# Optimization experiments

Measured on AMD Instinct MI355X. Metric: run time of the kernel, lower is better.

## Reference

```python
import jax, jax.numpy as jnp
import numpy as np

N_NODES = 4096
N_EDGES = 8192
N_GRAPHS = 256
D_NODE = 64
D_EDGE = 32
H = 256


def setup_inputs() -> dict:
    key = jax.random.key(0)
    ks = jax.random.split(key, 16)
    s = lambda d: 1.0 / np.sqrt(d)
    inp = {
        "x": jax.random.normal(ks[0], (N_NODES, D_NODE), dtype=jnp.float32),
        "edge_index": jax.random.randint(ks[1], (2, N_EDGES), 0, N_NODES),
        "edge_attr": jax.random.normal(ks[2], (N_EDGES, D_EDGE), dtype=jnp.float32),
        "batch": jnp.sort(jax.random.randint(ks[3], (N_NODES,), 0, N_GRAPHS)),
        # conv1: edge MLP 32 -> 64*256, root weight 64->256, bias 256
        "nn1_w": jax.random.normal(ks[4], (D_EDGE, D_NODE * H), dtype=jnp.float32) * s(D_EDGE),
        "nn1_b": jnp.zeros((D_NODE * H,), dtype=jnp.float32),
        "root1_w": jax.random.normal(ks[5], (D_NODE, H), dtype=jnp.float32) * s(D_NODE),
        "bias1": jnp.zeros((H,), dtype=jnp.float32),
        # conv2: edge MLP 32 -> 256*256, root weight 256->256, bias 256
        "nn2_w": jax.random.normal(ks[6], (D_EDGE, H * H), dtype=jnp.float32) * s(D_EDGE),
        "nn2_b": jnp.zeros((H * H,), dtype=jnp.float32),
        "root2_w": jax.random.normal(ks[7], (H, H), dtype=jnp.float32) * s(H),
        "bias2": jnp.zeros((H,), dtype=jnp.float32),
        # readout MLP: 256 -> 128 -> 1
        "lin1_w": jax.random.normal(ks[8], (H, H // 2), dtype=jnp.float32) * s(H),
        "lin1_b": jnp.zeros((H // 2,), dtype=jnp.float32),
        "lin2_w": jax.random.normal(ks[9], (H // 2, 1), dtype=jnp.float32) * s(H // 2),
        "lin2_b": jnp.zeros((1,), dtype=jnp.float32),
    }
    return inp


def nnconv(x, src, dst, edge_attr, nn_w, nn_b, root_w, bias, out_c):
    # PyG NNConv (aggr='add'): per-edge weight matrix from edge MLP,
    # message = x[src] @ W_e, scatter-add at dst, plus root transform + bias.
    e = edge_attr.shape[0]
    in_c = x.shape[1]
    w_e = (edge_attr @ nn_w + nn_b).reshape(e, in_c, out_c)  # [E, in, out]
    msg = jnp.einsum('ei,eio->eo', x[src], w_e)              # [E, out]
    agg = jax.ops.segment_sum(msg, dst, num_segments=x.shape[0])
    return agg + x @ root_w + bias


def reference(x, edge_index, edge_attr, batch,
              nn1_w, nn1_b, root1_w, bias1,
              nn2_w, nn2_b, root2_w, bias2,
              lin1_w, lin1_b, lin2_w, lin2_b):
    src, dst = edge_index[0], edge_index[1]
    h = nnconv(x, src, dst, edge_attr, nn1_w, nn1_b, root1_w, bias1, H)
    h = jax.nn.relu(h)
    h = nnconv(h, src, dst, edge_attr, nn2_w, nn2_b, root2_w, bias2, H)
    # global mean pool over graphs
    sums = jax.ops.segment_sum(h, batch, num_segments=N_GRAPHS)
    cnts = jax.ops.segment_sum(jnp.ones((h.shape[0],), h.dtype), batch, num_segments=N_GRAPHS)
    pooled = sums / jnp.maximum(cnts, 1.0)[:, None]
    # dropout is identity in eval mode
    z = jax.nn.relu(pooled @ lin1_w + lin1_b)
    return jax.nn.sigmoid(z @ lin2_w + lin2_b)  # [N_GRAPHS, 1]
```

## Files before the change

### kernel.cpp

```cpp
#include <hip/hip_runtime.h>
#include <math.h>

#define N_NODES 4096
#define N_EDGES 8192
#define N_GRAPHS 256
#define D_NODE 64
#define D_EDGE 32
#define HH 256

#define K1 2176
#define K2 8704
#define NC1 34
#define NC2 136
#define NSL1 8
#define NSL3 32
#define CHUNK 128

typedef _Float16 half8v __attribute__((ext_vector_type(8)));
typedef _Float16 half4v __attribute__((ext_vector_type(4)));
typedef float floatx4 __attribute__((ext_vector_type(4)));

static const size_t OFF_S    = 0;
static const size_t OFF_BT1  = 17825792;
static const size_t OFF_BT2  = 18104320;
static const size_t OFF_CP   = 19218432;
static const size_t OFF_H    = 25509888;
static const size_t OFF_INT  = 26034176;

__device__ void csr_body(const int* __restrict__ dst,
                         int* __restrict__ starts,
                         int* __restrict__ elist) {
    __shared__ int cnt[4096];
    __shared__ int ps[256];
    int t = threadIdx.x;
#pragma unroll
    for (int i = 0; i < 16; ++i) cnt[t * 16 + i] = 0;
    __syncthreads();
#pragma unroll
    for (int i = 0; i < 32; ++i) atomicAdd(&cnt[dst[i * 256 + t]], 1);
    __syncthreads();
    int v[16]; int s = 0;
#pragma unroll
    for (int i = 0; i < 16; ++i) { v[i] = cnt[t * 16 + i]; s += v[i]; }
    ps[t] = s;
    __syncthreads();
    for (int off = 1; off < 256; off <<= 1) {
        int tv = (t >= off) ? ps[t - off] : 0;
        __syncthreads();
        ps[t] += tv;
        __syncthreads();
    }
    int excl = ps[t] - s;
#pragma unroll
    for (int i = 0; i < 16; ++i) {
        starts[t * 16 + i] = excl;
        cnt[t * 16 + i] = excl;
        excl += v[i];
    }
    if (t == 255) starts[4096] = excl;
    __syncthreads();
#pragma unroll
    for (int i = 0; i < 32; ++i) {
        int e = i * 256 + t;
        int d = dst[e];
        int p = atomicAdd(&cnt[d], 1);
        elist[p] = e;
    }
}

__device__ void packT_body(const float* __restrict__ w,
                           const float* __restrict__ b,
                           const float* __restrict__ rw,
                           _Float16* __restrict__ BT,
                           int kk0, int o0, int K,
                           int wlim, int blim, int wshift, int wmask, int wrow) {
    __shared__ float T[64][65];
    int t = threadIdx.x;
    int ol = t & 63, kb = t >> 6;
#pragma unroll
    for (int p = 0; p < 16; ++p) {
        int kl = p * 4 + kb;
        int kk = kk0 + kl, o = o0 + ol;
        float v;
        if (kk < wlim)      v = w[(kk >> wshift) * wrow + (kk & wmask) * 256 + o];
        else if (kk < blim) v = b[(kk - wlim) * 256 + o];
        else                v = rw[(kk - blim) * 256 + o];
        T[kl][ol] = v;
    }
    __syncthreads();
    int kl2 = t & 63, ob = t >> 6;
#pragma unroll
    for (int p = 0; p < 16; ++p) {
        int ol2 = p * 4 + ob;
        BT[(size_t)(o0 + ol2) * K + kk0 + kl2] = (_Float16)T[kl2][ol2];
    }
}

__global__ __launch_bounds__(256) void prep_k(const int* __restrict__ dst,
                                              int* __restrict__ starts,
                                              int* __restrict__ elist,
                                              const float* __restrict__ w1,
                                              const float* __restrict__ b1,
                                              const float* __restrict__ r1,
                                              const float* __restrict__ w2,
                                              const float* __restrict__ b2,
                                              const float* __restrict__ r2,
                                              _Float16* __restrict__ BT1,
                                              _Float16* __restrict__ BT2) {
    int bx = blockIdx.x, by = blockIdx.y;
    if (bx == 0) {
        if (by == 0) csr_body(dst, starts, elist);
        return;
    }
    int pbx = bx - 1, o0 = by * 64;
    if (pbx < NC1)
        packT_body(w1, b1, r1, BT1, pbx * 64, o0, K1, 2048, 2112, 6, 63, 16384);
    else
        packT_body(w2, b2, r2, BT2, (pbx - NC1) * 64, o0, K2, 8192, 8448, 8, 255, 65536);
}

__global__ __launch_bounds__(64) void s1_k(const float* __restrict__ x,
                                           const float* __restrict__ ea,
                                           const int* __restrict__ src,
                                           const int* __restrict__ starts,
                                           const int* __restrict__ elist,
                                           _Float16* __restrict__ S) {
    int n = blockIdx.x, t = threadIdx.x;
    int cg = t & 7, kg = t >> 3;
    int i0 = cg * 8;
    float acc[5][8] = {};
    int e0 = starts[n], e1 = starts[n + 1];
    for (int ie = e0; ie < e1; ++ie) {
        int e = elist[ie];
        int sn = src[e];
        float4 f0 = *(const float4*)&x[sn * 64 + i0];
        float4 f1 = *(const float4*)&x[sn * 64 + i0 + 4];
        float xv[8] = {f0.x, f0.y, f0.z, f0.w, f1.x, f1.y, f1.z, f1.w};
#pragma unroll
        for (int j = 0; j < 4; ++j) {
            float va = ea[e * 32 + kg + 8 * j];
#pragma unroll
            for (int c = 0; c < 8; ++c) acc[j][c] += va * xv[c];
        }
        if (kg == 0) {
#pragma unroll
            for (int c = 0; c < 8; ++c) acc[4][c] += xv[c];
        }
    }
    _Float16* row = S + (size_t)n * K1;
#pragma unroll
    for (int j = 0; j < 4; ++j) {
        int k = kg + 8 * j;
        half8v o;
#pragma unroll
        for (int c = 0; c < 8; ++c) o[c] = (_Float16)acc[j][c];
        *(half8v*)&row[k * 64 + i0] = o;
    }
    if (kg == 0) {
        half8v o;
#pragma unroll
        for (int c = 0; c < 8; ++c) o[c] = (_Float16)acc[4][c];
        *(half8v*)&row[32 * 64 + i0] = o;
    }
    if (kg == 1) {
        float4 f0 = *(const float4*)&x[n * 64 + i0];
        float4 f1 = *(const float4*)&x[n * 64 + i0 + 4];
        half8v o;
        o[0] = (_Float16)f0.x; o[1] = (_Float16)f0.y; o[2] = (_Float16)f0.z; o[3] = (_Float16)f0.w;
        o[4] = (_Float16)f1.x; o[5] = (_Float16)f1.y; o[6] = (_Float16)f1.z; o[7] = (_Float16)f1.w;
        *(half8v*)&row[2112 + i0] = o;
    }
}

__device__ __forceinline__ void async_copy16(const void* g, void* l) {
    __builtin_amdgcn_global_load_lds(
        (__attribute__((address_space(1))) unsigned int*)(g),
        (__attribute__((address_space(3))) unsigned int*)(l), 16, 0, 0);
}

__global__ __launch_bounds__(256, 3) void gemm_f16(const _Float16* __restrict__ A,
                                                   const _Float16* __restrict__ BT,
                                                   _Float16* __restrict__ Cpart,
                                                   int K, int NC, int Z) {
    __shared__ _Float16 lds[17408];
    _Float16* As = lds;
    _Float16* Bs = lds + 128 * 64;
    int tid = threadIdx.x;
    int w = tid >> 6, l = tid & 63;
    int mt = blockIdx.y, nt = blockIdx.x, z = blockIdx.z;
    int c0 = z * NC / Z, c1 = (z + 1) * NC / Z;
    int k0 = c0 * 64;
    int wm = w & 1, wn = w >> 1;

    int lr = l >> 3, lc = l & 7;
    int gc = lc ^ lr;
    const _Float16* gA0 = A  + (size_t)(mt * 128 + w * 32 + lr) * K + k0 + gc * 8;
    const _Float16* gB0 = BT + (size_t)(nt * 128 + w * 32 + lr) * K + k0 + gc * 8;

    int lm = l & 15, q4 = l >> 4;
    int sw = lm & 7;

    floatx4 acc[4][4] = {};

    for (int s = c0; s < c1; ++s) {
#pragma unroll
        for (int q = 0; q < 4; ++q) {
            async_copy16(gA0 + (size_t)q * 8 * K, As + (w * 32 + q * 8) * 64);
            async_copy16(gB0 + (size_t)q * 8 * K, Bs + (w * 32 + q * 8) * 64);
        }
        gA0 += 64; gB0 += 64;
        __syncthreads();
#pragma unroll
        for (int kw = 0; kw < 2; ++kw) {
            int ck = ((kw * 4 + q4) ^ sw) * 8;
            half8v af[4], bf[4];
#pragma unroll
            for (int i = 0; i < 4; ++i)
                af[i] = *(const half8v*)&As[(wm * 64 + i * 16 + lm) * 64 + ck];
#pragma unroll
            for (int j = 0; j < 4; ++j)
                bf[j] = *(const half8v*)&Bs[(wn * 64 + j * 16 + lm) * 64 + ck];
#pragma unroll
            for (int i = 0; i < 4; ++i)
#pragma unroll
                for (int j = 0; j < 4; ++j)
                    acc[i][j] = __builtin_amdgcn_mfma_f32_16x16x32_f16(af[i], bf[j], acc[i][j], 0, 0, 0);
        }
        __syncthreads();
    }

    _Float16* ep = lds + w * 4352;
#pragma unroll
    for (int i = 0; i < 4; ++i)
#pragma unroll
        for (int j = 0; j < 4; ++j)
#pragma unroll
            for (int r = 0; r < 4; ++r)
                ep[(i * 16 + q4 * 4 + r) * 68 + j * 16 + lm] = (_Float16)acc[i][j][r];
    __syncthreads();
    _Float16* Cp = Cpart + (size_t)z * (N_NODES * HH);
    int row8 = l >> 3, colg = (l & 7) * 8;
    int gm0 = mt * 128 + wm * 64, gn0 = nt * 128 + wn * 64;
#pragma unroll
    for (int i8 = 0; i8 < 8; ++i8) {
        int rr = i8 * 8 + row8;
        half4v lo = *(const half4v*)&ep[rr * 68 + colg];
        half4v hi = *(const half4v*)&ep[rr * 68 + colg + 4];
        half8v v;
        v[0] = lo[0]; v[1] = lo[1]; v[2] = lo[2]; v[3] = lo[3];
        v[4] = hi[0]; v[5] = hi[1]; v[6] = hi[2]; v[7] = hi[3];
        *(half8v*)&Cp[(size_t)(gm0 + rr) * HH + gn0 + colg] = v;
    }
}

__global__ __launch_bounds__(256) void hep_k(const _Float16* __restrict__ Cp,
                                             const float* __restrict__ bias,
                                             _Float16* __restrict__ h) {
    int idx = (blockIdx.x * 256 + threadIdx.x) * 8;
    float a[8] = {};
#pragma unroll
    for (int zz = 0; zz < NSL1; ++zz) {
        half8v v = *(const half8v*)(Cp + (size_t)zz * (N_NODES * HH) + idx);
#pragma unroll
        for (int j = 0; j < 8; ++j) a[j] += (float)v[j];
    }
    int col = idx & 255;
    half8v o;
#pragma unroll
    for (int j = 0; j < 8; ++j) o[j] = (_Float16)fmaxf(a[j] + bias[col + j], 0.f);
    *(half8v*)(h + idx) = o;
}

__global__ __launch_bounds__(256) void sg_k(const _Float16* __restrict__ h,
                                            const float* __restrict__ ea,
                                            const int* __restrict__ src,
                                            const int* __restrict__ starts,
                                            const int* __restrict__ elist,
                                            const int* __restrict__ batch,
                                            _Float16* __restrict__ SG) {
    int g = blockIdx.x, kg = blockIdx.y, t = threadIdx.x;
    __shared__ int bnds[2];
    __shared__ int sl[CHUNK];
    __shared__ int el[CHUNK];
    if (t < 2) {
        int target = g + t;
        int lo = 0, hi = N_NODES;
        while (lo < hi) { int mid = (lo + hi) >> 1; if (batch[mid] < target) lo = mid + 1; else hi = mid; }
        bnds[t] = lo;
    }
    __syncthreads();
    int nlo = bnds[0], nhi = bnds[1];
    int e0 = starts[nlo], e1 = starts[nhi];
    _Float16* row = SG + (size_t)g * K2;

    if (kg < 8) {
        float acc[4] = {};
        for (int base = e0; base < e1; base += CHUNK) {
            int ne = min(CHUNK, e1 - base);
            if (t < ne) { int e = elist[base + t]; el[t] = e; sl[t] = src[e]; }
            __syncthreads();
            int ie = 0;
            for (; ie + 8 <= ne; ie += 8) {
                float hv[8]; float4 ev[8];
#pragma unroll
                for (int u = 0; u < 8; ++u) hv[u] = (float)h[(size_t)sl[ie + u] * 256 + t];
#pragma unroll
                for (int u = 0; u < 8; ++u) ev[u] = *(const float4*)&ea[(size_t)el[ie + u] * 32 + kg * 4];
#pragma unroll
                for (int u = 0; u < 8; ++u) {
                    acc[0] += ev[u].x * hv[u]; acc[1] += ev[u].y * hv[u];
                    acc[2] += ev[u].z * hv[u]; acc[3] += ev[u].w * hv[u];
                }
            }
            for (; ie < ne; ++ie) {
                float hv = (float)h[(size_t)sl[ie] * 256 + t];
                float4 ev = *(const float4*)&ea[(size_t)el[ie] * 32 + kg * 4];
                acc[0] += ev.x * hv; acc[1] += ev.y * hv;
                acc[2] += ev.z * hv; acc[3] += ev.w * hv;
            }
            __syncthreads();
        }
#pragma unroll
        for (int j = 0; j < 4; ++j)
            row[(kg * 4 + j) * 256 + t] = (_Float16)acc[j];
    } else {
        float a32 = 0.f;
        for (int base = e0; base < e1; base += CHUNK) {
            int ne = min(CHUNK, e1 - base);
            if (t < ne) sl[t] = src[elist[base + t]];
            __syncthreads();
            int ie = 0;
            for (; ie + 8 <= ne; ie += 8) {
                float hv[8];
#pragma unroll
                for (int u = 0; u < 8; ++u) hv[u] = (float)h[(size_t)sl[ie + u] * 256 + t];
#pragma unroll
                for (int u = 0; u < 8; ++u) a32 += hv[u];
            }
            for (; ie < ne; ++ie)
                a32 += (float)h[(size_t)sl[ie] * 256 + t];
            __syncthreads();
        }
        float aug = 0.f;
        int n = nlo;
        for (; n + 4 <= nhi; n += 4) {
            float hv[4];
#pragma unroll
            for (int u = 0; u < 4; ++u) hv[u] = (float)h[(size_t)(n + u) * 256 + t];
#pragma unroll
            for (int u = 0; u < 4; ++u) aug += hv[u];
        }
        for (; n < nhi; ++n) aug += (float)h[(size_t)n * 256 + t];
        row[32 * 256 + t] = (_Float16)a32;
        row[8448 + t] = (_Float16)aug;
    }
}

__global__ __launch_bounds__(256, 3) void gemm_sg(const _Float16* __restrict__ A,
                                                  const _Float16* __restrict__ BT,
                                                  float* __restrict__ Cp,
                                                  int K, int NC, int Z) {
    __shared__ _Float16 lds[16384];
    _Float16* As = lds;
    _Float16* Bs = lds + 128 * 64;
    int tid = threadIdx.x;
    int w = tid >> 6, l = tid & 63;
    int mt = blockIdx.y, nt = blockIdx.x, z = blockIdx.z;
    int c0 = z * NC / Z, c1 = (z + 1) * NC / Z;
    int k0 = c0 * 64;
    int wm = w & 1, wn = w >> 1;

    int lr = l >> 3, lc = l & 7;
    int gc = lc ^ lr;
    const _Float16* gA0 = A  + (size_t)(mt * 128 + w * 32 + lr) * K + k0 + gc * 8;
    const _Float16* gB0 = BT + (size_t)(nt * 128 + w * 32 + lr) * K + k0 + gc * 8;

    int lm = l & 15, q4 = l >> 4;
    int sw = lm & 7;

    floatx4 acc[4][4] = {};

    for (int s = c0; s < c1; ++s) {
#pragma unroll
        for (int q = 0; q < 4; ++q) {
            async_copy16(gA0 + (size_t)q * 8 * K, As + (w * 32 + q * 8) * 64);
            async_copy16(gB0 + (size_t)q * 8 * K, Bs + (w * 32 + q * 8) * 64);
        }
        gA0 += 64; gB0 += 64;
        __syncthreads();
#pragma unroll
        for (int kw = 0; kw < 2; ++kw) {
            int ck = ((kw * 4 + q4) ^ sw) * 8;
            half8v af[4], bf[4];
#pragma unroll
            for (int i = 0; i < 4; ++i)
                af[i] = *(const half8v*)&As[(wm * 64 + i * 16 + lm) * 64 + ck];
#pragma unroll
            for (int j = 0; j < 4; ++j)
                bf[j] = *(const half8v*)&Bs[(wn * 64 + j * 16 + lm) * 64 + ck];
#pragma unroll
            for (int i = 0; i < 4; ++i)
#pragma unroll
                for (int j = 0; j < 4; ++j)
                    acc[i][j] = __builtin_amdgcn_mfma_f32_16x16x32_f16(af[i], bf[j], acc[i][j], 0, 0, 0);
        }
        __syncthreads();
    }

    float* C = Cp + (size_t)z * (N_GRAPHS * HH);
    int gm0 = mt * 128 + wm * 64, gn0 = nt * 128 + wn * 64;
#pragma unroll
    for (int i = 0; i < 4; ++i)
#pragma unroll
        for (int j = 0; j < 4; ++j)
#pragma unroll
            for (int r = 0; r < 4; ++r)
                C[(size_t)(gm0 + i * 16 + q4 * 4 + r) * HH + gn0 + j * 16 + lm] = acc[i][j][r];
}

__global__ __launch_bounds__(256) void readout_k(const float* __restrict__ CpS,
                                                 const int* __restrict__ batch,
                                                 const float* __restrict__ bias2,
                                                 const float* __restrict__ l1w,
                                                 const float* __restrict__ l1b,
                                                 const float* __restrict__ l2w,
                                                 const float* __restrict__ l2b,
                                                 float* __restrict__ out) {
    int g = blockIdx.x, t = threadIdx.x;
    __shared__ int bnds[2];
    __shared__ float sp[256];
    __shared__ float sz[128];
    if (t < 2) {
        int target = g + t;
        int lo = 0, hi = N_NODES;
        while (lo < hi) { int mid = (lo + hi) >> 1; if (batch[mid] < target) lo = mid + 1; else hi = mid; }
        bnds[t] = lo;
    }
    __syncthreads();
    int lo = bnds[0], hi = bnds[1];
    float s = 0.f;
#pragma unroll
    for (int zz = 0; zz < NSL3; ++zz)
        s += CpS[(size_t)zz * (N_GRAPHS * HH) + g * 256 + t];
    sp[t] = (hi > lo) ? (s / (float)(hi - lo) + bias2[t]) : 0.f;
    __syncthreads();
    if (t < 128) {
        float a = l1b[t];
#pragma unroll 8
        for (int i = 0; i < 256; ++i) a += sp[i] * l1w[i * 128 + t];
        sz[t] = fmaxf(a, 0.f) * l2w[t];
    }
    __syncthreads();
    for (int ss = 64; ss > 0; ss >>= 1) {
        if (t < ss) sz[t] += sz[t + ss];
        __syncthreads();
    }
    if (t == 0) {
        float zz = sz[0] + l2b[0];
        out[g] = 1.0f / (1.0f + expf(-zz));
    }
}

extern "C" void kernel_launch(void* const* d_in, const int* in_sizes, int n_in,
                              void* d_out, int out_size, void* d_ws, size_t ws_size,
                              hipStream_t stream) {
    const float* x       = (const float*)d_in[0];
    const int*   ei      = (const int*)d_in[1];
    const float* ea      = (const float*)d_in[2];
    const int*   batch   = (const int*)d_in[3];
    const float* nn1_w   = (const float*)d_in[4];
    const float* nn1_b   = (const float*)d_in[5];
    const float* root1_w = (const float*)d_in[6];
    const float* bias1   = (const float*)d_in[7];
    const float* nn2_w   = (const float*)d_in[8];
    const float* nn2_b   = (const float*)d_in[9];
    const float* root2_w = (const float*)d_in[10];
    const float* bias2   = (const float*)d_in[11];
    const float* lin1_w  = (const float*)d_in[12];
    const float* lin1_b  = (const float*)d_in[13];
    const float* lin2_w  = (const float*)d_in[14];
    const float* lin2_b  = (const float*)d_in[15];
    float* out = (float*)d_out;
    float* ws  = (float*)d_ws;

    _Float16* S   = (_Float16*)(ws + OFF_S);
    _Float16* BT1 = (_Float16*)(ws + OFF_BT1);
    _Float16* BT2 = (_Float16*)(ws + OFF_BT2);
    _Float16* Cp  = (_Float16*)(ws + OFF_CP);
    float*    CpS = ws + OFF_CP;
    _Float16* h   = (_Float16*)(ws + OFF_H);
    int* ip     = (int*)(ws + OFF_INT);
    int* starts = ip;
    int* elist  = ip + 4100;

    const int* srcv = ei;
    const int* dstv = ei + N_EDGES;

    prep_k<<<dim3(1 + NC1 + NC2, 4), 256, 0, stream>>>(
        dstv, starts, elist, nn1_w, nn1_b, root1_w, nn2_w, nn2_b, root2_w, BT1, BT2);

    s1_k<<<4096, 64, 0, stream>>>(x, ea, srcv, starts, elist, S);

    gemm_f16<<<dim3(2, 32, NSL1), 256, 0, stream>>>(S, BT1, Cp, K1, NC1, NSL1);

    hep_k<<<512, 256, 0, stream>>>(Cp, bias1, h);

    sg_k<<<dim3(N_GRAPHS, 9), 256, 0, stream>>>(h, ea, srcv, starts, elist, batch, S);

    gemm_sg<<<dim3(2, 2, NSL3), 256, 0, stream>>>(S, BT2, CpS, K2, NC2, NSL3);

    readout_k<<<N_GRAPHS, 256, 0, stream>>>(CpS, batch, bias2,
                                            lin1_w, lin1_b, lin2_w, lin2_b, out);
}
```

Measured before the change: 173.6 us.

## Precompute graph bounds, atomically pool gemm_sg output, restructure sg_k and s1_k blocks

Graph start offsets are now computed once in the prep kernel instead of by binary search in sg_k and readout_k. gemm_sg accumulates its split-K partials directly into a pool buffer with atomicAdd, with the buffer zeroed in hep_k, so the 32-slice partial buffer and its reduction in readout_k go away. sg_k now runs 2 k-slices instead of 9. Each block stages edge attributes in shared memory with a smaller chunk and accumulates 16 columns per thread. s1_k packs four nodes per 256-thread block. The trade-offs are float atomic contention and nondeterministic summation order, plus fewer blocks and higher register pressure in sg_k.

```diff
diff --git a/kernel.cpp b/kernel.cpp
--- a/kernel.cpp
+++ b/kernel.cpp
@@ -14,7 +14,7 @@
 #define NC2 136
 #define NSL1 8
 #define NSL3 32
-#define CHUNK 128
+#define CHUNK 64
 
 typedef _Float16 half8v __attribute__((ext_vector_type(8)));
 typedef _Float16 half4v __attribute__((ext_vector_type(4)));
@@ -26,6 +26,7 @@
 static const size_t OFF_CP   = 19218432;
 static const size_t OFF_H    = 25509888;
 static const size_t OFF_INT  = 26034176;
+static const size_t OFF_POOL = 26050560;
 
 __device__ void csr_body(const int* __restrict__ dst,
                          int* __restrict__ starts,
@@ -66,6 +67,14 @@
         int p = atomicAdd(&cnt[d], 1);
         elist[p] = e;
     }
+}
+
+__device__ void gstarts_body(const int* __restrict__ batch, int* __restrict__ gstarts) {
+    int t = threadIdx.x;
+    int lo = 0, hi = N_NODES;
+    while (lo < hi) { int mid = (lo + hi) >> 1; if (batch[mid] < t) lo = mid + 1; else hi = mid; }
+    gstarts[t] = lo;
+    if (t == 0) gstarts[N_GRAPHS] = N_NODES;
 }
 
 __device__ void packT_body(const float* __restrict__ w,
@@ -97,8 +106,10 @@
 }
 
 __global__ __launch_bounds__(256) void prep_k(const int* __restrict__ dst,
+                                              const int* __restrict__ batch,
                                               int* __restrict__ starts,
                                               int* __restrict__ elist,
+                                              int* __restrict__ gstarts,
                                               const float* __restrict__ w1,
                                               const float* __restrict__ b1,
                                               const float* __restrict__ r1,
@@ -110,6 +121,7 @@
     int bx = blockIdx.x, by = blockIdx.y;
     if (bx == 0) {
         if (by == 0) csr_body(dst, starts, elist);
+        else if (by == 1) gstarts_body(batch, gstarts);
         return;
     }
     int pbx = bx - 1, o0 = by * 64;
@@ -119,14 +131,16 @@
         packT_body(w2, b2, r2, BT2, (pbx - NC1) * 64, o0, K2, 8192, 8448, 8, 255, 65536);
 }
 
-__global__ __launch_bounds__(64) void s1_k(const float* __restrict__ x,
-                                           const float* __restrict__ ea,
-                                           const int* __restrict__ src,
-                                           const int* __restrict__ starts,
-                                           const int* __restrict__ elist,
-                                           _Float16* __restrict__ S) {
-    int n = blockIdx.x, t = threadIdx.x;
-    int cg = t & 7, kg = t >> 3;
+__global__ __launch_bounds__(256) void s1_k(const float* __restrict__ x,
+                                            const float* __restrict__ ea,
+                                            const int* __restrict__ src,
+                                            const int* __restrict__ starts,
+                                            const int* __restrict__ elist,
+                                            _Float16* __restrict__ S) {
+    int t = threadIdx.x;
+    int n = blockIdx.x * 4 + (t >> 6);
+    int tl = t & 63;
+    int cg = tl & 7, kg = tl >> 3;
     int i0 = cg * 8;
     float acc[5][8] = {};
     int e0 = starts[n], e1 = starts[n + 1];
@@ -255,7 +269,9 @@
 
 __global__ __launch_bounds__(256) void hep_k(const _Float16* __restrict__ Cp,
                                              const float* __restrict__ bias,
-                                             _Float16* __restrict__ h) {
+                                             _Float16* __restrict__ h,
+                                             float* __restrict__ pool) {
+    if (blockIdx.x < 256) pool[blockIdx.x * 256 + threadIdx.x] = 0.f;
     int idx = (blockIdx.x * 256 + threadIdx.x) * 8;
     float a[8] = {};
 #pragma unroll
@@ -276,71 +292,60 @@
                                             const int* __restrict__ src,
                                             const int* __restrict__ starts,
                                             const int* __restrict__ elist,
-                                            const int* __restrict__ batch,
+                                            const int* __restrict__ gstarts,
                                             _Float16* __restrict__ SG) {
-    int g = blockIdx.x, kg = blockIdx.y, t = threadIdx.x;
-    __shared__ int bnds[2];
+    int g = blockIdx.x, ks = blockIdx.y, t = threadIdx.x;
     __shared__ int sl[CHUNK];
     __shared__ int el[CHUNK];
-    if (t < 2) {
-        int target = g + t;
-        int lo = 0, hi = N_NODES;
-        while (lo < hi) { int mid = (lo + hi) >> 1; if (batch[mid] < target) lo = mid + 1; else hi = mid; }
-        bnds[t] = lo;
-    }
-    __syncthreads();
-    int nlo = bnds[0], nhi = bnds[1];
+    __shared__ float eaS[CHUNK * 32];
+    int nlo = gstarts[g], nhi = gstarts[g + 1];
     int e0 = starts[nlo], e1 = starts[nhi];
     _Float16* row = SG + (size_t)g * K2;
-
-    if (kg < 8) {
-        float acc[4] = {};
-        for (int base = e0; base < e1; base += CHUNK) {
-            int ne = min(CHUNK, e1 - base);
-            if (t < ne) { int e = elist[base + t]; el[t] = e; sl[t] = src[e]; }
-            __syncthreads();
-            int ie = 0;
-            for (; ie + 8 <= ne; ie += 8) {
-                float hv[8]; float4 ev[8];
-#pragma unroll
-                for (int u = 0; u < 8; ++u) hv[u] = (float)h[(size_t)sl[ie + u] * 256 + t];
-#pragma unroll
-                for (int u = 0; u < 8; ++u) ev[u] = *(const float4*)&ea[(size_t)el[ie + u] * 32 + kg * 4];
-#pragma unroll
-                for (int u = 0; u < 8; ++u) {
-                    acc[0] += ev[u].x * hv[u]; acc[1] += ev[u].y * hv[u];
-                    acc[2] += ev[u].z * hv[u]; acc[3] += ev[u].w * hv[u];
+    int kbase = ks * 16;
+
+    float acc[16] = {};
+    float a32 = 0.f;
+    for (int base = e0; base < e1; base += CHUNK) {
+        int ne = min(CHUNK, e1 - base);
+        if (t < ne) { int e = elist[base + t]; el[t] = e; sl[t] = src[e]; }
+        __syncthreads();
+        for (int j = t; j < ne * 32; j += 256)
+            eaS[j] = ea[(size_t)el[j >> 5] * 32 + (j & 31)];
+        __syncthreads();
+        int ie = 0;
+        for (; ie + 4 <= ne; ie += 4) {
+            float hv[4];
+#pragma unroll
+            for (int u = 0; u < 4; ++u) hv[u] = (float)h[(size_t)sl[ie + u] * 256 + t];
+#pragma unroll
+            for (int u = 0; u < 4; ++u) {
+                const float* er = &eaS[(ie + u) * 32 + kbase];
+#pragma unroll
+                for (int q = 0; q < 4; ++q) {
+                    float4 ev = *(const float4*)&er[q * 4];
+                    acc[q * 4 + 0] += ev.x * hv[u]; acc[q * 4 + 1] += ev.y * hv[u];
+                    acc[q * 4 + 2] += ev.z * hv[u]; acc[q * 4 + 3] += ev.w * hv[u];
                 }
+                if (ks == 1) a32 += hv[u];
             }
-            for (; ie < ne; ++ie) {
-                float hv = (float)h[(size_t)sl[ie] * 256 + t];
-                float4 ev = *(const float4*)&ea[(size_t)el[ie] * 32 + kg * 4];
-                acc[0] += ev.x * hv; acc[1] += ev.y * hv;
-                acc[2] += ev.z * hv; acc[3] += ev.w * hv;
+        }
+        for (; ie < ne; ++ie) {
+            float hv = (float)h[(size_t)sl[ie] * 256 + t];
+            const float* er = &eaS[ie * 32 + kbase];
+#pragma unroll
+            for (int q = 0; q < 4; ++q) {
+                float4 ev = *(const float4*)&er[q * 4];
+                acc[q * 4 + 0] += ev.x * hv; acc[q * 4 + 1] += ev.y * hv;
+                acc[q * 4 + 2] += ev.z * hv; acc[q * 4 + 3] += ev.w * hv;
             }
-            __syncthreads();
-        }
-#pragma unroll
-        for (int j = 0; j < 4; ++j)
-            row[(kg * 4 + j) * 256 + t] = (_Float16)acc[j];
-    } else {
-        float a32 = 0.f;
-        for (int base = e0; base < e1; base += CHUNK) {
-            int ne = min(CHUNK, e1 - base);
-            if (t < ne) sl[t] = src[elist[base + t]];
-            __syncthreads();
-            int ie = 0;
-            for (; ie + 8 <= ne; ie += 8) {
-                float hv[8];
-#pragma unroll
-                for (int u = 0; u < 8; ++u) hv[u] = (float)h[(size_t)sl[ie + u] * 256 + t];
-#pragma unroll
-                for (int u = 0; u < 8; ++u) a32 += hv[u];
-            }
-            for (; ie < ne; ++ie)
-                a32 += (float)h[(size_t)sl[ie] * 256 + t];
-            __syncthreads();
-        }
+            if (ks == 1) a32 += hv;
+        }
+        __syncthreads();
+    }
+#pragma unroll
+    for (int j = 0; j < 16; ++j)
+        row[(kbase + j) * 256 + t] = (_Float16)acc[j];
+    if (ks == 1) {
         float aug = 0.f;
         int n = nlo;
         for (; n + 4 <= nhi; n += 4) {
@@ -358,7 +363,7 @@
 
 __global__ __launch_bounds__(256, 3) void gemm_sg(const _Float16* __restrict__ A,
                                                   const _Float16* __restrict__ BT,
-                                                  float* __restrict__ Cp,
+                                                  float* __restrict__ pool,
                                                   int K, int NC, int Z) {
     __shared__ _Float16 lds[16384];
     _Float16* As = lds;
@@ -407,7 +412,6 @@
         __syncthreads();
     }
 
-    float* C = Cp + (size_t)z * (N_GRAPHS * HH);
     int gm0 = mt * 128 + wm * 64, gn0 = nt * 128 + wn * 64;
 #pragma unroll
     for (int i = 0; i < 4; ++i)
@@ -415,11 +419,12 @@
         for (int j = 0; j < 4; ++j)
 #pragma unroll
             for (int r = 0; r < 4; ++r)
-                C[(size_t)(gm0 + i * 16 + q4 * 4 + r) * HH + gn0 + j * 16 + lm] = acc[i][j][r];
-}
-
-__global__ __launch_bounds__(256) void readout_k(const float* __restrict__ CpS,
-                                                 const int* __restrict__ batch,
+                atomicAdd(&pool[(size_t)(gm0 + i * 16 + q4 * 4 + r) * HH + gn0 + j * 16 + lm],
+                          acc[i][j][r]);
+}
+
+__global__ __launch_bounds__(256) void readout_k(const float* __restrict__ pool,
+                                                 const int* __restrict__ gstarts,
                                                  const float* __restrict__ bias2,
                                                  const float* __restrict__ l1w,
                                                  const float* __restrict__ l1b,
@@ -427,22 +432,10 @@
                                                  const float* __restrict__ l2b,
                                                  float* __restrict__ out) {
     int g = blockIdx.x, t = threadIdx.x;
-    __shared__ int bnds[2];
     __shared__ float sp[256];
     __shared__ float sz[128];
-    if (t < 2) {
-        int target = g + t;
-        int lo = 0, hi = N_NODES;
-        while (lo < hi) { int mid = (lo + hi) >> 1; if (batch[mid] < target) lo = mid + 1; else hi = mid; }
-        bnds[t] = lo;
-    }
-    __syncthreads();
-    int lo = bnds[0], hi = bnds[1];
-    float s = 0.f;
-#pragma unroll
-    for (int zz = 0; zz < NSL3; ++zz)
-        s += CpS[(size_t)zz * (N_GRAPHS * HH) + g * 256 + t];
-    sp[t] = (hi > lo) ? (s / (float)(hi - lo) + bias2[t]) : 0.f;
+    int lo = gstarts[g], hi = gstarts[g + 1];
+    sp[t] = (hi > lo) ? (pool[g * 256 + t] / (float)(hi - lo) + bias2[t]) : 0.f;
     __syncthreads();
     if (t < 128) {
         float a = l1b[t];
@@ -487,28 +480,30 @@
     _Float16* BT1 = (_Float16*)(ws + OFF_BT1);
     _Float16* BT2 = (_Float16*)(ws + OFF_BT2);
     _Float16* Cp  = (_Float16*)(ws + OFF_CP);
-    float*    CpS = ws + OFF_CP;
     _Float16* h   = (_Float16*)(ws + OFF_H);
-    int* ip     = (int*)(ws + OFF_INT);
-    int* starts = ip;
-    int* elist  = ip + 4100;
+    int* ip      = (int*)(ws + OFF_INT);
+    int* starts  = ip;
+    int* elist   = ip + 4100;
+    int* gstarts = ip + 12292;
+    float* pool  = ws + OFF_POOL;
 
     const int* srcv = ei;
     const int* dstv = ei + N_EDGES;
 
     prep_k<<<dim3(1 + NC1 + NC2, 4), 256, 0, stream>>>(
-        dstv, starts, elist, nn1_w, nn1_b, root1_w, nn2_w, nn2_b, root2_w, BT1, BT2);
-
-    s1_k<<<4096, 64, 0, stream>>>(x, ea, srcv, starts, elist, S);
+        dstv, batch, starts, elist, gstarts,
+        nn1_w, nn1_b, root1_w, nn2_w, nn2_b, root2_w, BT1, BT2);
+
+    s1_k<<<1024, 256, 0, stream>>>(x, ea, srcv, starts, elist, S);
 
     gemm_f16<<<dim3(2, 32, NSL1), 256, 0, stream>>>(S, BT1, Cp, K1, NC1, NSL1);
 
-    hep_k<<<512, 256, 0, stream>>>(Cp, bias1, h);
-
-    sg_k<<<dim3(N_GRAPHS, 9), 256, 0, stream>>>(h, ea, srcv, starts, elist, batch, S);
-
-    gemm_sg<<<dim3(2, 2, NSL3), 256, 0, stream>>>(S, BT2, CpS, K2, NC2, NSL3);
-
-    readout_k<<<N_GRAPHS, 256, 0, stream>>>(CpS, batch, bias2,
+    hep_k<<<512, 256, 0, stream>>>(Cp, bias1, h, pool);
+
+    sg_k<<<dim3(N_GRAPHS, 2), 256, 0, stream>>>(h, ea, srcv, starts, elist, gstarts, S);
+
+    gemm_sg<<<dim3(2, 2, NSL3), 256, 0, stream>>>(S, BT2, pool, K2, NC2, NSL3);
+
+    readout_k<<<N_GRAPHS, 256, 0, stream>>>(pool, gstarts, bias2,
                                             lin1_w, lin1_b, lin2_w, lin2_b, out);
 }
```

New measurement: 168.4 us, median of 2. 1.03x faster.
